# Kernel optimization log

Hardware: AMD Instinct MI355X
Metric: run time of the kernel (lower is better)

The kernel has to match this reference:

```python
import jax, jax.numpy as jnp
import numpy as np

N, L, S, H, D = 2, 2048, 2048, 8, 64

def elu_feature_map(x):
    return jax.nn.elu(x) + 1.0

def setup_inputs() -> dict:
    key = jax.random.key(0)
    k1, k2, k3, k4, k5 = jax.random.split(key, 5)
    return {
        "queries": jax.random.normal(k1, (N, L, H, D), dtype=jnp.float32),
        "keys": jax.random.normal(k2, (N, S, H, D), dtype=jnp.float32),
        "values": jax.random.normal(k3, (N, S, H, D), dtype=jnp.float32),
        "q_mask": jnp.ones((N, L), dtype=jnp.float32),
        "kv_mask": jnp.ones((N, S), dtype=jnp.float32),
        "W": jax.random.normal(k4, (1, 2), dtype=jnp.float32) * 0.5,  # nn.Linear(2,1) weight
        "b": jax.random.normal(k5, (1,), dtype=jnp.float32) * 0.5,    # nn.Linear(2,1) bias
    }

def reference(queries, keys, values, q_mask, kv_mask, W, b):
    # feature map: elu(x) + 1
    Q = elu_feature_map(queries) * q_mask[:, :, None, None]   # [N,L,H,D]
    K = elu_feature_map(keys) * kv_mask[:, :, None, None]     # [N,S,H,D]
    queries_m = queries * q_mask[:, :, None, None]
    values_m = values * kv_mask[:, :, None, None]  # masked but unused downstream (as in original)
    del values_m
    # full QK score tensor [N,L,S,H]
    qk = jnp.einsum('nlhd,nshd->nlsh', Q, K)
    qk_mean = jnp.mean(qk, axis=2)  # [N,L,H]
    qk_max = jnp.max(qk, axis=2)    # [N,L,H]
    stats = jnp.stack([qk_mean, qk_max], axis=-1)  # [N,L,H,2]
    gate = jax.nn.sigmoid(jnp.einsum('nlhe,oe->nlho', stats, W) + b)  # [N,L,H,1]
    atten = gate[..., 0]  # [N,L,H]
    return queries_m * atten[..., None]  # [N,L,H,D]
```

## Files before the change

kernel.cpp:

```cpp
#include <hip/hip_runtime.h>
#include <math.h>

#define N_ 2
#define L_ 2048
#define S_ 2048
#define H_ 8
#define D_ 64

#define BLK_L 256
#define BS 64
#define SSPLIT 4
#define KPAD 72

typedef __attribute__((ext_vector_type(8))) short short8;
typedef __attribute__((ext_vector_type(4))) float floatx4;

__device__ __forceinline__ float feat(float x) {
    return x > 0.0f ? x + 1.0f : __expf(x);
}
__device__ __forceinline__ short f2bf(float x) {
    unsigned u = __float_as_uint(x);
    unsigned r = (u + 0x7fffu + ((u >> 16) & 1u)) >> 16;
    return (short)r;
}
__device__ __forceinline__ float bf2f(short h) {
    return __uint_as_float(((unsigned)(unsigned short)h) << 16);
}

__global__ __launch_bounds__(256) void ksum_kernel(const float* __restrict__ K,
        const float* __restrict__ kvmask, float* __restrict__ Ksum) {
    int nh = blockIdx.x;
    int z = blockIdx.y;
    int n = nh >> 3, h = nh & 7;
    int t = threadIdx.x;
    int d = t & 63, sc = t >> 6;
    float sum = 0.f;
    int s0 = z * 64 + sc * 16;
    #pragma unroll
    for (int k = 0; k < 16; ++k) {
        int s = s0 + k;
        float v = K[(((size_t)n * S_ + s) * H_ + h) * D_ + d];
        sum += feat(v) * kvmask[n * S_ + s];
    }
    __shared__ float sm[256];
    sm[t] = sum;
    __syncthreads();
    if (t < 64) {
        float tot = sm[t] + sm[t + 64] + sm[t + 128] + sm[t + 192];
        atomicAdd(&Ksum[nh * 64 + t], tot);
    }
}

__global__ __launch_bounds__(256) void rowmax_mfma(
        const float* __restrict__ Q, const float* __restrict__ K,
        const float* __restrict__ qmask, const float* __restrict__ kvmask,
        float* __restrict__ rowmaxg) {
    __shared__ short Kh[BS * KPAD];
    __shared__ short Kl[BS * KPAD];

    int nh = blockIdx.y;
    int n = nh >> 3, h = nh & 7;
    int t = threadIdx.x;
    int w = t >> 6, lane = t & 63;
    int quad = lane >> 4, l16 = lane & 15;
    int lblock = blockIdx.x * BLK_L;
    int z = blockIdx.z;

    short8 Ah[4][2], Al[4][2];
    #pragma unroll
    for (int lsub = 0; lsub < 4; ++lsub) {
        int lrow = lblock + w * 64 + lsub * 16 + l16;
        float qm = qmask[n * L_ + lrow];
        const float* qp = Q + (((size_t)n * L_ + lrow) * H_ + h) * D_ + quad * 8;
        #pragma unroll
        for (int ks = 0; ks < 2; ++ks) {
            float4 v0 = *(const float4*)(qp + ks * 32);
            float4 v1 = *(const float4*)(qp + ks * 32 + 4);
            float fv[8];
            fv[0] = feat(v0.x) * qm; fv[1] = feat(v0.y) * qm;
            fv[2] = feat(v0.z) * qm; fv[3] = feat(v0.w) * qm;
            fv[4] = feat(v1.x) * qm; fv[5] = feat(v1.y) * qm;
            fv[6] = feat(v1.z) * qm; fv[7] = feat(v1.w) * qm;
            short8 hi, lo;
            #pragma unroll
            for (int j = 0; j < 8; ++j) {
                short hb = f2bf(fv[j]);
                hi[j] = hb;
                lo[j] = f2bf(fv[j] - bf2f(hb));
            }
            Ah[lsub][ks] = hi;
            Al[lsub][ks] = lo;
        }
    }

    float rmax[4][4];
    #pragma unroll
    for (int i = 0; i < 4; ++i)
        #pragma unroll
        for (int r = 0; r < 4; ++r) rmax[i][r] = 0.f;

    const int tiles = S_ / SSPLIT / BS;
    for (int tile = 0; tile < tiles; ++tile) {
        int sbase = z * (S_ / SSPLIT) + tile * BS;
        __syncthreads();
        {
            int row = t >> 2, chunk = t & 3;
            float km = kvmask[n * S_ + sbase + row];
            const float* kp = K + (((size_t)n * S_ + sbase + row) * H_ + h) * D_ + chunk * 16;
            float fv[16];
            #pragma unroll
            for (int j = 0; j < 4; ++j) {
                float4 v = *(const float4*)(kp + j * 4);
                fv[4 * j + 0] = feat(v.x) * km;
                fv[4 * j + 1] = feat(v.y) * km;
                fv[4 * j + 2] = feat(v.z) * km;
                fv[4 * j + 3] = feat(v.w) * km;
            }
            short8 h0, h1, l0, l1;
            #pragma unroll
            for (int j = 0; j < 8; ++j) {
                short hb = f2bf(fv[j]);
                h0[j] = hb;
                l0[j] = f2bf(fv[j] - bf2f(hb));
                short hb2 = f2bf(fv[8 + j]);
                h1[j] = hb2;
                l1[j] = f2bf(fv[8 + j] - bf2f(hb2));
            }
            short* dh = &Kh[row * KPAD + chunk * 16];
            short* dl = &Kl[row * KPAD + chunk * 16];
            *(short8*)(dh)     = h0;
            *(short8*)(dh + 8) = h1;
            *(short8*)(dl)     = l0;
            *(short8*)(dl + 8) = l1;
        }
        __syncthreads();

        #pragma unroll
        for (int ssub = 0; ssub < 4; ++ssub) {
            const short* bph = &Kh[(ssub * 16 + l16) * KPAD + quad * 8];
            const short* bpl = &Kl[(ssub * 16 + l16) * KPAD + quad * 8];
            short8 Bh0 = *(const short8*)(bph);
            short8 Bh1 = *(const short8*)(bph + 32);
            short8 Bl0 = *(const short8*)(bpl);
            short8 Bl1 = *(const short8*)(bpl + 32);
            #pragma unroll
            for (int lsub = 0; lsub < 4; ++lsub) {
                floatx4 acc = {0.f, 0.f, 0.f, 0.f};
                acc = __builtin_amdgcn_mfma_f32_16x16x32_bf16(Ah[lsub][0], Bh0, acc, 0, 0, 0);
                acc = __builtin_amdgcn_mfma_f32_16x16x32_bf16(Ah[lsub][1], Bh1, acc, 0, 0, 0);
                acc = __builtin_amdgcn_mfma_f32_16x16x32_bf16(Ah[lsub][0], Bl0, acc, 0, 0, 0);
                acc = __builtin_amdgcn_mfma_f32_16x16x32_bf16(Ah[lsub][1], Bl1, acc, 0, 0, 0);
                acc = __builtin_amdgcn_mfma_f32_16x16x32_bf16(Al[lsub][0], Bh0, acc, 0, 0, 0);
                acc = __builtin_amdgcn_mfma_f32_16x16x32_bf16(Al[lsub][1], Bh1, acc, 0, 0, 0);
                #pragma unroll
                for (int r = 0; r < 4; ++r)
                    rmax[lsub][r] = fmaxf(rmax[lsub][r], acc[r]);
            }
        }
    }

    #pragma unroll
    for (int lsub = 0; lsub < 4; ++lsub)
        #pragma unroll
        for (int r = 0; r < 4; ++r) {
            float m = rmax[lsub][r];
            m = fmaxf(m, __shfl_xor(m, 1, 64));
            m = fmaxf(m, __shfl_xor(m, 2, 64));
            m = fmaxf(m, __shfl_xor(m, 4, 64));
            m = fmaxf(m, __shfl_xor(m, 8, 64));
            if (l16 == 0) {
                int l = lblock + w * 64 + lsub * 16 + quad * 4 + r;
                atomicMax((unsigned*)&rowmaxg[(size_t)nh * L_ + l],
                          __float_as_uint(m));
            }
        }
}

__global__ __launch_bounds__(256) void finalize_kernel(
        const float* __restrict__ Q, const float* __restrict__ qmask,
        const float* __restrict__ Ksum, const float* __restrict__ rowmaxg,
        const float* __restrict__ W, const float* __restrict__ b,
        float* __restrict__ out) {
    int t = threadIdx.x;
    int lane = t & 63;
    int wid = (blockIdx.x << 2) | (t >> 6);
    int n = wid / (L_ * H_);
    int lh = wid % (L_ * H_);
    int l = lh / H_, h = lh % H_;

    float q = Q[(size_t)wid * 64 + lane];
    float qm = qmask[n * L_ + l];
    float p = feat(q) * qm * Ksum[(n * H_ + h) * 64 + lane];
    #pragma unroll
    for (int off = 32; off > 0; off >>= 1)
        p += __shfl_xor(p, off, 64);
    float mean = p * (1.0f / S_);
    float mx = rowmaxg[((size_t)n * H_ + h) * L_ + l];
    float zz = W[0] * mean + W[1] * mx + b[0];
    float g = 1.0f / (1.0f + __expf(-zz));
    out[(size_t)wid * 64 + lane] = q * qm * g;
}

extern "C" void kernel_launch(void* const* d_in, const int* in_sizes, int n_in,
                              void* d_out, int out_size, void* d_ws, size_t ws_size,
                              hipStream_t stream) {
    const float* Q      = (const float*)d_in[0];
    const float* K      = (const float*)d_in[1];
    const float* qmask  = (const float*)d_in[3];
    const float* kvmask = (const float*)d_in[4];
    const float* W      = (const float*)d_in[5];
    const float* b      = (const float*)d_in[6];
    float* out = (float*)d_out;

    float* Ksum   = (float*)d_ws;
    float* rowmax = (float*)d_ws + 1024;

    hipMemsetAsync(Ksum, 0, 1024 * sizeof(float), stream);
    hipMemsetAsync(rowmax, 0, (size_t)N_ * H_ * L_ * sizeof(float), stream);

    ksum_kernel<<<dim3(N_ * H_, 32), 256, 0, stream>>>(K, kvmask, Ksum);
    rowmax_mfma<<<dim3(L_ / BLK_L, N_ * H_, SSPLIT), 256, 0, stream>>>(
        Q, K, qmask, kvmask, rowmax);
    finalize_kernel<<<dim3(N_ * L_ * H_ / 4), 256, 0, stream>>>(
        Q, qmask, Ksum, rowmax, W, b, out);
}
```

Baseline: 122.9 us.

## Precompute bf16 hi/lo K once and double-buffer it via global_load_lds

Moves the K feature map and bf16 hi/lo split out of the rowmax kernel into a prepass kernel. That kernel writes swizzled hi/lo arrays to workspace and also produces Ksum. The rowmax kernel then streams those tiles into double-buffered LDS with async global_load_lds, overlapping loads with MFMA work and dropping the redundant per-block conversion. Block indices are remapped so that blocks sharing K data are scheduled together, and the two memsets are merged. The cost is extra global traffic for the bf16 arrays and a larger workspace.

```diff
diff --git a/kernel.cpp b/kernel.cpp
--- a/kernel.cpp
+++ b/kernel.cpp
@@ -10,7 +10,6 @@
 #define BLK_L 256
 #define BS 64
 #define SSPLIT 4
-#define KPAD 72
 
 typedef __attribute__((ext_vector_type(8))) short short8;
 typedef __attribute__((ext_vector_type(4))) float floatx4;
@@ -26,45 +25,96 @@
 __device__ __forceinline__ float bf2f(short h) {
     return __uint_as_float(((unsigned)(unsigned short)h) << 16);
 }
-
-__global__ __launch_bounds__(256) void ksum_kernel(const float* __restrict__ K,
-        const float* __restrict__ kvmask, float* __restrict__ Ksum) {
+__device__ __forceinline__ void gload_lds16(const void* g, void* l) {
+    __builtin_amdgcn_global_load_lds(
+        (__attribute__((address_space(1))) void*)g,
+        (__attribute__((address_space(3))) void*)l, 16, 0, 0);
+}
+
+__global__ __launch_bounds__(256) void featk_kernel(
+        const float* __restrict__ K, const float* __restrict__ kvmask,
+        short* __restrict__ Khi, short* __restrict__ Klo,
+        float* __restrict__ Ksum) {
+    __shared__ float sm[64][68];
     int nh = blockIdx.x;
-    int z = blockIdx.y;
+    int z  = blockIdx.y;
     int n = nh >> 3, h = nh & 7;
     int t = threadIdx.x;
-    int d = t & 63, sc = t >> 6;
-    float sum = 0.f;
-    int s0 = z * 64 + sc * 16;
-    #pragma unroll
-    for (int k = 0; k < 16; ++k) {
-        int s = s0 + k;
-        float v = K[(((size_t)n * S_ + s) * H_ + h) * D_ + d];
-        sum += feat(v) * kvmask[n * S_ + s];
-    }
-    __shared__ float sm[256];
-    sm[t] = sum;
+    int srow = t >> 2, g = t & 3;
+    int s = z * 64 + srow;
+
+    float km = kvmask[n * S_ + s];
+    const float* kp = K + (((size_t)n * S_ + s) * H_ + h) * D_ + g * 16;
+    float fv[16];
+    #pragma unroll
+    for (int j = 0; j < 4; ++j) {
+        float4 v = *(const float4*)(kp + j * 4);
+        fv[4 * j + 0] = feat(v.x) * km;
+        fv[4 * j + 1] = feat(v.y) * km;
+        fv[4 * j + 2] = feat(v.z) * km;
+        fv[4 * j + 3] = feat(v.w) * km;
+    }
+    short8 h0, h1, l0, l1;
+    #pragma unroll
+    for (int j = 0; j < 8; ++j) {
+        short hb = f2bf(fv[j]);
+        h0[j] = hb;  l0[j] = f2bf(fv[j] - bf2f(hb));
+        short hb2 = f2bf(fv[8 + j]);
+        h1[j] = hb2; l1[j] = f2bf(fv[8 + j] - bf2f(hb2));
+    }
+    size_t rowbase = ((size_t)nh * S_ + s) * (size_t)D_;
+    int rx = srow & 7;
+    *(short8*)(Khi + rowbase + ((((2 * g)    ) ^ rx) << 3)) = h0;
+    *(short8*)(Khi + rowbase + ((((2 * g) + 1) ^ rx) << 3)) = h1;
+    *(short8*)(Klo + rowbase + ((((2 * g)    ) ^ rx) << 3)) = l0;
+    *(short8*)(Klo + rowbase + ((((2 * g) + 1) ^ rx) << 3)) = l1;
+
+    #pragma unroll
+    for (int j2 = 0; j2 < 4; ++j2)
+        *(float4*)&sm[srow][g * 16 + 4 * j2] =
+            make_float4(fv[4 * j2], fv[4 * j2 + 1], fv[4 * j2 + 2], fv[4 * j2 + 3]);
     __syncthreads();
     if (t < 64) {
-        float tot = sm[t] + sm[t + 64] + sm[t + 128] + sm[t + 192];
+        float tot = 0.f;
+        #pragma unroll
+        for (int r = 0; r < 64; ++r) tot += sm[r][t];
         atomicAdd(&Ksum[nh * 64 + t], tot);
     }
 }
 
 __global__ __launch_bounds__(256) void rowmax_mfma(
-        const float* __restrict__ Q, const float* __restrict__ K,
-        const float* __restrict__ qmask, const float* __restrict__ kvmask,
+        const float* __restrict__ Q, const short* __restrict__ Khi,
+        const short* __restrict__ Klo, const float* __restrict__ qmask,
         float* __restrict__ rowmaxg) {
-    __shared__ short Kh[BS * KPAD];
-    __shared__ short Kl[BS * KPAD];
-
-    int nh = blockIdx.y;
+    __shared__ __align__(16) char lds[2][16384];
+
+    int flat = blockIdx.x + (blockIdx.y << 3) + (blockIdx.z << 7);
+    int nid  = ((flat & 7) << 6) | (flat >> 3);
+    int bx = nid & 7;
+    int nh = (nid >> 3) & 15;
+    int z  = nid >> 7;
+
     int n = nh >> 3, h = nh & 7;
     int t = threadIdx.x;
     int w = t >> 6, lane = t & 63;
     int quad = lane >> 4, l16 = lane & 15;
-    int lblock = blockIdx.x * BLK_L;
-    int z = blockIdx.z;
+    int lblock = bx * BLK_L;
+
+    const char* gKh = (const char*)Khi + ((size_t)nh * S_ + (size_t)z * (S_ / SSPLIT)) * 128;
+    const char* gKl = (const char*)Klo + ((size_t)nh * S_ + (size_t)z * (S_ / SSPLIT)) * 128;
+    int sidx = w << 2;
+
+    auto stage = [&](int tile, int db) {
+        #pragma unroll
+        for (int c = 0; c < 4; ++c) {
+            int idx = sidx | c;
+            const char* src = (idx < 8 ? gKh : gKl)
+                              + tile * 8192 + ((idx & 7) << 10) + (lane << 4);
+            gload_lds16(src, &lds[db][idx << 10]);
+        }
+    };
+
+    stage(0, 0);
 
     short8 Ah[4][2], Al[4][2];
     #pragma unroll
@@ -93,56 +143,35 @@
         }
     }
 
+    int boff[4][2];
+    #pragma unroll
+    for (int ssub = 0; ssub < 4; ++ssub) {
+        int row = ssub * 16 + l16;
+        int rx = l16 & 7;
+        boff[ssub][0] = row * 128 + ((quad ^ rx) << 4);
+        boff[ssub][1] = row * 128 + (((quad + 4) ^ rx) << 4);
+    }
+
     float rmax[4][4];
     #pragma unroll
     for (int i = 0; i < 4; ++i)
         #pragma unroll
         for (int r = 0; r < 4; ++r) rmax[i][r] = 0.f;
+
+    __syncthreads();
 
     const int tiles = S_ / SSPLIT / BS;
     for (int tile = 0; tile < tiles; ++tile) {
-        int sbase = z * (S_ / SSPLIT) + tile * BS;
-        __syncthreads();
-        {
-            int row = t >> 2, chunk = t & 3;
-            float km = kvmask[n * S_ + sbase + row];
-            const float* kp = K + (((size_t)n * S_ + sbase + row) * H_ + h) * D_ + chunk * 16;
-            float fv[16];
-            #pragma unroll
-            for (int j = 0; j < 4; ++j) {
-                float4 v = *(const float4*)(kp + j * 4);
-                fv[4 * j + 0] = feat(v.x) * km;
-                fv[4 * j + 1] = feat(v.y) * km;
-                fv[4 * j + 2] = feat(v.z) * km;
-                fv[4 * j + 3] = feat(v.w) * km;
-            }
-            short8 h0, h1, l0, l1;
-            #pragma unroll
-            for (int j = 0; j < 8; ++j) {
-                short hb = f2bf(fv[j]);
-                h0[j] = hb;
-                l0[j] = f2bf(fv[j] - bf2f(hb));
-                short hb2 = f2bf(fv[8 + j]);
-                h1[j] = hb2;
-                l1[j] = f2bf(fv[8 + j] - bf2f(hb2));
-            }
-            short* dh = &Kh[row * KPAD + chunk * 16];
-            short* dl = &Kl[row * KPAD + chunk * 16];
-            *(short8*)(dh)     = h0;
-            *(short8*)(dh + 8) = h1;
-            *(short8*)(dl)     = l0;
-            *(short8*)(dl + 8) = l1;
-        }
-        __syncthreads();
-
+        int db = tile & 1;
+        if (tile + 1 < tiles) stage(tile + 1, db ^ 1);
+        const char* hp = lds[db];
+        const char* lp = lds[db] + 8192;
         #pragma unroll
         for (int ssub = 0; ssub < 4; ++ssub) {
-            const short* bph = &Kh[(ssub * 16 + l16) * KPAD + quad * 8];
-            const short* bpl = &Kl[(ssub * 16 + l16) * KPAD + quad * 8];
-            short8 Bh0 = *(const short8*)(bph);
-            short8 Bh1 = *(const short8*)(bph + 32);
-            short8 Bl0 = *(const short8*)(bpl);
-            short8 Bl1 = *(const short8*)(bpl + 32);
+            short8 Bh0 = *(const short8*)(hp + boff[ssub][0]);
+            short8 Bh1 = *(const short8*)(hp + boff[ssub][1]);
+            short8 Bl0 = *(const short8*)(lp + boff[ssub][0]);
+            short8 Bl1 = *(const short8*)(lp + boff[ssub][1]);
             #pragma unroll
             for (int lsub = 0; lsub < 4; ++lsub) {
                 floatx4 acc = {0.f, 0.f, 0.f, 0.f};
@@ -157,6 +186,7 @@
                     rmax[lsub][r] = fmaxf(rmax[lsub][r], acc[r]);
             }
         }
+        __syncthreads();
     }
 
     #pragma unroll
@@ -214,13 +244,14 @@
 
     float* Ksum   = (float*)d_ws;
     float* rowmax = (float*)d_ws + 1024;
-
-    hipMemsetAsync(Ksum, 0, 1024 * sizeof(float), stream);
-    hipMemsetAsync(rowmax, 0, (size_t)N_ * H_ * L_ * sizeof(float), stream);
-
-    ksum_kernel<<<dim3(N_ * H_, 32), 256, 0, stream>>>(K, kvmask, Ksum);
+    short* Khi    = (short*)((float*)d_ws + 1024 + 32768);
+    short* Klo    = Khi + (size_t)N_ * H_ * S_ * D_;
+
+    hipMemsetAsync(d_ws, 0, (1024 + (size_t)N_ * H_ * L_) * sizeof(float), stream);
+
+    featk_kernel<<<dim3(N_ * H_, S_ / 64), 256, 0, stream>>>(K, kvmask, Khi, Klo, Ksum);
     rowmax_mfma<<<dim3(L_ / BLK_L, N_ * H_, SSPLIT), 256, 0, stream>>>(
-        Q, K, qmask, kvmask, rowmax);
+        Q, Khi, Klo, qmask, rowmax);
     finalize_kernel<<<dim3(N_ * L_ * H_ / 4), 256, 0, stream>>>(
         Q, qmask, Ksum, rowmax, W, b, out);
 }
```

Result: faster. 115.4 us (-6.1%).
